# Kernel tuning notes

Measured on AMD Instinct MI355X. Metric: run time of the kernel, lower is better.

## Reference

```python
import jax, jax.numpy as jnp
import numpy as np

B = 16
Dv, Hv, Wv = 128, 128, 128   # patchsize voxel grid (C=1)
NPTS = 1920                  # 16*120 points
EPS_IN = 1e-5                # InstanceNorm eps


def _inorm(x):
    # InstanceNorm1d, affine=False: normalize over last (length) dim per (b, c)
    m = jnp.mean(x, axis=-1, keepdims=True)
    v = jnp.var(x, axis=-1, keepdims=True)
    return (x - m) * jax.lax.rsqrt(v + EPS_IN)


def _mlp(q, w1, b1, w2, b2, w3, b3, w4, b4, w5, b5):
    b = q.shape[0]
    x = q.reshape(b, 256, 8)                                    # (b, 2048//8, 8)
    x = jnp.einsum('bil,oi->bol', x, w1) + b1[None, :, None]    # Conv1d(256,240,1) -> (b,240,8)
    x = jax.nn.relu(_inorm(x.reshape(b, 64, 30)))               # view (b,64,30), IN(64)
    # Conv1d(64,128,1,groups=64): each in-ch -> 2 out-chs; then view (b,32,120)
    x = (x[:, :, None, :] * w2[None, :, :, None] + b2.reshape(1, 64, 2, 1)).reshape(b, 32, 120)
    x = jax.nn.relu(_inorm(x))
    # Conv1d(32,64,1,groups=32); view (b,16,480)
    x = (x[:, :, None, :] * w3[None, :, :, None] + b3.reshape(1, 32, 2, 1)).reshape(b, 16, 480)
    x = jax.nn.relu(_inorm(x))
    # Conv1d(16,64,1,groups=16); view (b,16,1920)
    x = (x[:, :, None, :] * w4[None, :, :, None] + b4.reshape(1, 16, 4, 1)).reshape(b, 16, 1920)
    x = jax.nn.relu(_inorm(x))
    return jnp.einsum('bil,oi->bol', x, w5) + b5[None, :, None]  # Conv1d(16,3,1) -> (b,3,1920)


def _splat(vals, grid):
    # True adjoint of 3D grid_sample (align_corners=False, zeros padding):
    # trilinear scatter-add of point values into the voxel grid.
    # vals: (b, N); grid: (b, N, 3) with (x, y, z) ~ (W, H, D) normalized coords.
    b, n = vals.shape
    px = ((grid[..., 0] + 1.0) * Wv - 1.0) * 0.5
    py = ((grid[..., 1] + 1.0) * Hv - 1.0) * 0.5
    pz = ((grid[..., 2] + 1.0) * Dv - 1.0) * 0.5
    x0f = jnp.floor(px); y0f = jnp.floor(py); z0f = jnp.floor(pz)
    fx = px - x0f; fy = py - y0f; fz = pz - z0f
    x0 = x0f.astype(jnp.int32); y0 = y0f.astype(jnp.int32); z0 = z0f.astype(jnp.int32)
    bidx = jnp.arange(b, dtype=jnp.int32)[:, None]
    out = jnp.zeros(b * Dv * Hv * Wv, dtype=vals.dtype)
    for dz in (0, 1):
        wz = fz if dz else (1.0 - fz)
        for dy in (0, 1):
            wy = fy if dy else (1.0 - fy)
            for dx in (0, 1):
                wx = fx if dx else (1.0 - fx)
                xi = x0 + dx; yi = y0 + dy; zi = z0 + dz
                w = wx * wy * wz * vals
                valid = (xi >= 0) & (xi < Wv) & (yi >= 0) & (yi < Hv) & (zi >= 0) & (zi < Dv)
                w = jnp.where(valid, w, 0.0)
                xi = jnp.clip(xi, 0, Wv - 1)
                yi = jnp.clip(yi, 0, Hv - 1)
                zi = jnp.clip(zi, 0, Dv - 1)
                flat = ((bidx * Dv + zi) * Hv + yi) * Wv + xi
                out = out.at[flat.ravel()].add(w.ravel())
    return out.reshape(b, 1, Dv, Hv, Wv)


def _avgpool3(x):
    # AvgPool3d(3, stride=1, padding=1, count_include_pad=True) as separable 1D averages
    for ax in (2, 3, 4):
        pad = [(1, 1) if i == ax else (0, 0) for i in range(5)]
        xp = jnp.pad(x, pad)
        n = x.shape[ax]
        x = (jax.lax.slice_in_dim(xp, 0, n, axis=ax)
             + jax.lax.slice_in_dim(xp, 1, n + 1, axis=ax)
             + jax.lax.slice_in_dim(xp, 2, n + 2, axis=ax)) / 3.0
    return x


def _smooth(x):
    return _avgpool3(_avgpool3(_avgpool3(x)))


def _forward(q, q_val, w1, b1, w2, b2, w3, b3, w4, b4, w5, b5):
    b = q.shape[0]
    q3 = _mlp(q, w1, b1, w2, b2, w3, b3, w4, b4, w5, b5)   # (b, 3, 1920)
    coords = jnp.tanh(q3)                                    # q0_coord
    grid = jnp.transpose(coords, (0, 2, 1))                  # (b, 1920, 3)
    vals = jnp.broadcast_to(jax.nn.sigmoid(q_val).reshape(1, NPTS), (b, NPTS))
    out = _splat(vals, grid)
    out0 = _splat(jnp.ones((b, NPTS), q.dtype), grid)
    return _smooth(out) / (_smooth(out0) + 0.001)


def setup_inputs() -> dict:
    key = jax.random.key(0)
    ks = jax.random.split(key, 12)
    sc = 0.1
    return {
        'q': jax.random.normal(ks[0], (B, 2048), jnp.float32),
        'q_val': jax.random.normal(ks[1], (1, 1, 16, 120), jnp.float32),
        'w1': jax.random.normal(ks[2], (240, 256), jnp.float32) * sc,
        'b1': jax.random.normal(ks[3], (240,), jnp.float32) * sc,
        'w2': jax.random.normal(ks[4], (64, 2), jnp.float32) * sc,
        'b2': jax.random.normal(ks[5], (128,), jnp.float32) * sc,
        'w3': jax.random.normal(ks[6], (32, 2), jnp.float32) * sc,
        'b3': jax.random.normal(ks[7], (64,), jnp.float32) * sc,
        'w4': jax.random.normal(ks[8], (16, 4), jnp.float32) * sc,
        'b4': jax.random.normal(ks[9], (64,), jnp.float32) * sc,
        'w5': jax.random.normal(ks[10], (3, 16), jnp.float32) * sc,
        'b5': jax.random.normal(ks[11], (3,), jnp.float32) * sc,
    }


def reference(q, q_val, w1, b1, w2, b2, w3, b3, w4, b4, w5, b5):
    return _forward(q, q_val, w1, b1, w2, b2, w3, b3, w4, b4, w5, b5)
```

## Files before the change

kernel.cpp:

```cpp
#include <hip/hip_runtime.h>
#include <cstddef>

#define NB 16
#define NVOX 128
#define NPT 1920
#define NPAIRS 32768

static __device__ __forceinline__ float2 f2(float a, float b) {
    float2 r; r.x = a; r.y = b; return r;
}

__global__ __launch_bounds__(256)
void zero_out(float4* __restrict__ out)
{
    int idx = blockIdx.x * 2048 + threadIdx.x;
    #pragma unroll
    for (int i = 0; i < 8; ++i)
        out[idx + i * 256] = make_float4(0.f, 0.f, 0.f, 0.f);
}

__global__ __launch_bounds__(256)
void mlp_stage1(const float* __restrict__ q, const float* __restrict__ w1,
                const float* __restrict__ b1, float* __restrict__ x1g)
{
    __shared__ float wrow[256];
    __shared__ float psum[256];
    const int o = blockIdx.x;
    const int t = threadIdx.x;

    wrow[t] = w1[o * 256 + t];
    __syncthreads();

    const int half = t >> 7;
    const int bl = t & 127;
    const int b = bl >> 3, l = bl & 7;
    const float* qb = q + b * 2048 + l + half * 1024;
    float s = 0.f;
    #pragma unroll 8
    for (int i = 0; i < 128; ++i)
        s = fmaf(wrow[half * 128 + i], qb[i * 8], s);
    psum[t] = s;
    __syncthreads();

    if (t < 128) {
        int bb = t >> 3, ll = t & 7;
        x1g[bb * 1920 + o * 8 + ll] = b1[o] + psum[t] + psum[t + 128];
    }
}

__global__ __launch_bounds__(256)
void mlp_tail(const float* __restrict__ x1g, const float* __restrict__ qval,
              const float* __restrict__ w2, const float* __restrict__ b2,
              const float* __restrict__ w3, const float* __restrict__ b3,
              const float* __restrict__ w4, const float* __restrict__ b4,
              const float* __restrict__ w5, const float* __restrict__ b5,
              float4* __restrict__ pts, unsigned char* __restrict__ flags)
{
    __shared__ float bufA[7680];
    __shared__ float bufC[3840];
    __shared__ float psum[256], psq[256];
    __shared__ float meanv[64], rstdv[64];
    __shared__ float m4[16], r4[16];

    const int b = blockIdx.x;
    const int t = threadIdx.x;

    for (int u = t; u < 1920; u += 256) bufA[u] = x1g[b * 1920 + u];
    __syncthreads();

    {
        int c = t >> 2, g = t & 3;
        float s = 0.f, s2 = 0.f;
        for (int p = g; p < 30; p += 4) { float v = bufA[c * 30 + p]; s += v; s2 += v * v; }
        psum[t] = s; psq[t] = s2;
    }
    __syncthreads();
    if (t < 64) {
        float s = 0.f, s2 = 0.f;
        for (int g = 0; g < 4; ++g) { s += psum[t * 4 + g]; s2 += psq[t * 4 + g]; }
        float m = s * (1.f / 30.f);
        float var = s2 * (1.f / 30.f) - m * m;
        meanv[t] = m; rstdv[t] = rsqrtf(var + 1e-5f);
    }
    __syncthreads();
    for (int k = t; k < 1920; k += 256) {
        int c = k / 30;
        bufA[k] = fmaxf((bufA[k] - meanv[c]) * rstdv[c], 0.f);
    }
    __syncthreads();

    for (int m = t; m < 3840; m += 256) {
        int c = m / 60;
        int r = m - c * 60;
        int j = r / 30;
        int p = r - j * 30;
        bufC[m] = fmaf(bufA[c * 30 + p], w2[c * 2 + j], b2[c * 2 + j]);
    }
    __syncthreads();
    {
        int c = t >> 3, g = t & 7;
        float s = 0.f, s2 = 0.f;
        for (int p = g; p < 120; p += 8) { float v = bufC[c * 120 + p]; s += v; s2 += v * v; }
        psum[t] = s; psq[t] = s2;
    }
    __syncthreads();
    if (t < 32) {
        float s = 0.f, s2 = 0.f;
        for (int g = 0; g < 8; ++g) { s += psum[t * 8 + g]; s2 += psq[t * 8 + g]; }
        float m = s * (1.f / 120.f);
        float var = s2 * (1.f / 120.f) - m * m;
        meanv[t] = m; rstdv[t] = rsqrtf(var + 1e-5f);
    }
    __syncthreads();
    for (int m = t; m < 3840; m += 256) {
        int c = m / 120;
        bufC[m] = fmaxf((bufC[m] - meanv[c]) * rstdv[c], 0.f);
    }
    __syncthreads();

    for (int m = t; m < 7680; m += 256) {
        int c = m / 240;
        int r = m - c * 240;
        int j = r / 120;
        int p = r - j * 120;
        bufA[m] = fmaf(bufC[c * 120 + p], w3[c * 2 + j], b3[c * 2 + j]);
    }
    __syncthreads();

    const int c3 = t >> 4, g3 = t & 15;
    {
        float s = 0.f, s2 = 0.f;
        for (int k = 0; k < 30; ++k) { float v = bufA[c3 * 480 + g3 + 16 * k]; s += v; s2 += v * v; }
        psum[t] = s; psq[t] = s2;
    }
    __syncthreads();
    if (t < 16) {
        float s = 0.f, s2 = 0.f;
        for (int g = 0; g < 16; ++g) { s += psum[t * 16 + g]; s2 += psq[t * 16 + g]; }
        float m = s * (1.f / 480.f);
        float var = s2 * (1.f / 480.f) - m * m;
        meanv[t] = m; rstdv[t] = rsqrtf(var + 1e-5f);
    }
    __syncthreads();
    {
        float m = meanv[c3], r = rstdv[c3];
        float s = 0.f, s2 = 0.f;
        for (int k = 0; k < 30; ++k) {
            int idx = c3 * 480 + g3 + 16 * k;
            float v = fmaxf((bufA[idx] - m) * r, 0.f);
            bufA[idx] = v; s += v; s2 += v * v;
        }
        psum[t] = s; psq[t] = s2;
    }
    __syncthreads();
    if (t < 16) {
        float s = 0.f, s2 = 0.f;
        for (int g = 0; g < 16; ++g) { s += psum[t * 16 + g]; s2 += psq[t * 16 + g]; }
        float sum4 = 0.f, sq4 = 0.f;
        for (int j = 0; j < 4; ++j) {
            float w = w4[t * 4 + j], bb = b4[t * 4 + j];
            sum4 += w * s + 480.f * bb;
            sq4  += w * w * s2 + 2.f * w * bb * s + 480.f * bb * bb;
        }
        float m = sum4 * (1.f / 1920.f);
        float var = sq4 * (1.f / 1920.f) - m * m;
        m4[t] = m; r4[t] = rsqrtf(var + 1e-5f);
    }
    __syncthreads();

    for (int l = t; l < NPT; l += 256) {
        int j = l / 480;
        int p = l - j * 480;
        float a0 = b5[0], a1 = b5[1], a2 = b5[2];
        #pragma unroll
        for (int c = 0; c < 16; ++c) {
            float xv = bufA[c * 480 + p];
            float x4 = fmaf(xv, w4[c * 4 + j], b4[c * 4 + j]);
            float h  = fmaxf((x4 - m4[c]) * r4[c], 0.f);
            a0 = fmaf(w5[c],      h, a0);
            a1 = fmaf(w5[16 + c], h, a1);
            a2 = fmaf(w5[32 + c], h, a2);
        }
        float px = tanhf(a0) * 64.f + 63.5f;
        float py = tanhf(a1) * 64.f + 63.5f;
        float pz = tanhf(a2) * 64.f + 63.5f;
        float val = 1.f / (1.f + expf(-qval[l]));

        float4 pv; pv.x = px; pv.y = py; pv.z = pz; pv.w = val;
        pts[b * NPT + l] = pv;

        int x0 = (int)floorf(px), y0 = (int)floorf(py), z0 = (int)floorf(pz);
        int xlo = max(0, x0 - 3), xhi = min(127, x0 + 4);
        int ylo = max(0, y0 - 3), yhi = min(127, y0 + 4);
        int zlo = max(0, z0 - 3), zhi = min(127, z0 + 4);
        if (xlo > xhi || ylo > yhi || zlo > zhi) continue;
        int txl = xlo >> 3, txh = xhi >> 3;
        int tyl = ylo >> 3, tyh = yhi >> 3;
        int tzl = zlo >> 3, tzh = zhi >> 3;
        for (int tz = tzl; tz <= tzh; ++tz)
            for (int ty = tyl; ty <= tyh; ++ty)
                for (int tx = txl; tx <= txh; ++tx)
                    flags[((b * 16 + tz) * 16 + ty) * 16 + tx] = 1;
    }
}

__global__ __launch_bounds__(256)
void compact_tiles(const unsigned char* __restrict__ flags,
                   int* __restrict__ count, int* __restrict__ list)
{
    int i = blockIdx.x * 256 + threadIdx.x;
    const unsigned short* fp = (const unsigned short*)flags;
    if (fp[i] != 0) {
        int pos = atomicAdd(count, 1);
        list[pos] = i;
    }
}

__device__ __forceinline__ void coef(int g, float& cm1, float& c0, float& cp1)
{
    cm1 = (g == 1 || g == 127) ? 5.f : 6.f;
    c0  = (g == 0 || g == 127) ? 4.f : 7.f;
    cp1 = (g == 0 || g == 126) ? 5.f : 6.f;
}

__global__ __launch_bounds__(512)
void tile_active(const float4* __restrict__ pts, const int* __restrict__ count,
                 const int* __restrict__ list, float* __restrict__ out)
{
    __shared__ float2 raw[14 * 14 * 22];
    __shared__ float2 zs[8 * 14 * 22];

    if ((int)blockIdx.x >= *count) return;
    const int code = list[blockIdx.x];
    const int pair = code & 7;
    const int ty   = (code >> 3) & 15;
    const int tz   = (code >> 7) & 15;
    const int b    = code >> 11;
    const int Tx = pair * 16, Ty = ty * 8, Tz = tz * 8;
    const int t = threadIdx.x;

    float* ob = out + (((size_t)(b * NVOX + Tz) * NVOX + Ty) * NVOX + Tx);

    for (int u = t; u < 14 * 14 * 22; u += 512) raw[u] = f2(0.f, 0.f);
    __syncthreads();

    const float4* pb = pts + b * NPT;
    for (int p = t; p < NPT; p += 512) {
        float4 pt = pb[p];
        float x0f = floorf(pt.x), y0f = floorf(pt.y), z0f = floorf(pt.z);
        int x0 = (int)x0f, y0 = (int)y0f, z0 = (int)z0f;
        int lx0 = x0 - Tx + 3, ly0 = y0 - Ty + 3, lz0 = z0 - Tz + 3;
        if (lx0 + 1 < 0 || lx0 > 21 || ly0 + 1 < 0 || ly0 > 13 ||
            lz0 + 1 < 0 || lz0 > 13) continue;
        float fx = pt.x - x0f, fy = pt.y - y0f, fz = pt.z - z0f;
        float val = pt.w;
        #pragma unroll
        for (int dz = 0; dz < 2; ++dz) {
            int zi = z0 + dz, lz = lz0 + dz;
            if ((unsigned)zi >= 128u || (unsigned)lz >= 14u) continue;
            float wz = dz ? fz : 1.f - fz;
            #pragma unroll
            for (int dy = 0; dy < 2; ++dy) {
                int yi = y0 + dy, ly = ly0 + dy;
                if ((unsigned)yi >= 128u || (unsigned)ly >= 14u) continue;
                float wy = dy ? fy : 1.f - fy;
                #pragma unroll
                for (int dx = 0; dx < 2; ++dx) {
                    int xi = x0 + dx, lx = lx0 + dx;
                    if ((unsigned)xi >= 128u || (unsigned)lx >= 22u) continue;
                    float w = (dx ? fx : 1.f - fx) * wy * wz;
                    float2* cell = &raw[(lz * 14 + ly) * 22 + lx];
                    atomicAdd(&cell->x, w * val);
                    atomicAdd(&cell->y, w);
                }
            }
        }
    }
    __syncthreads();

    for (int u = t; u < 8 * 14 * 22; u += 512) {
        int lx = u % 22;
        int tmp = u / 22;
        int ly = tmp % 14;
        int lz = tmp / 14;
        float cm1, c0, cp1; coef(Tz + lz, cm1, c0, cp1);
        const float2* a = &raw[(lz * 14 + ly) * 22 + lx];
        const int S = 14 * 22;
        float sx = (a[0].x + a[6 * S].x) + 3.f * (a[S].x + a[5 * S].x)
                 + cm1 * a[2 * S].x + c0 * a[3 * S].x + cp1 * a[4 * S].x;
        float sy = (a[0].y + a[6 * S].y) + 3.f * (a[S].y + a[5 * S].y)
                 + cm1 * a[2 * S].y + c0 * a[3 * S].y + cp1 * a[4 * S].y;
        zs[u] = f2(sx * (1.f / 27.f), sy * (1.f / 27.f));
    }
    __syncthreads();

    float2* ys = raw;
    for (int u = t; u < 8 * 8 * 22; u += 512) {
        int lx = u % 22;
        int tmp = u / 22;
        int ly = tmp % 8;
        int lz = tmp / 8;
        float cm1, c0, cp1; coef(Ty + ly, cm1, c0, cp1);
        const float2* a = &zs[(lz * 14 + ly) * 22 + lx];
        const int S = 22;
        float sx = (a[0].x + a[6 * S].x) + 3.f * (a[S].x + a[5 * S].x)
                 + cm1 * a[2 * S].x + c0 * a[3 * S].x + cp1 * a[4 * S].x;
        float sy = (a[0].y + a[6 * S].y) + 3.f * (a[S].y + a[5 * S].y)
                 + cm1 * a[2 * S].y + c0 * a[3 * S].y + cp1 * a[4 * S].y;
        ys[(lz * 8 + ly) * 22 + lx] = f2(sx * (1.f / 27.f), sy * (1.f / 27.f));
    }
    __syncthreads();

    for (int u = t; u < 16 * 8 * 8; u += 512) {
        int x = u & 15, y = (u >> 4) & 7, z = u >> 7;
        float cm1, c0, cp1; coef(Tx + x, cm1, c0, cp1);
        const float2* a = &ys[(z * 8 + y) * 22 + x];
        float sx = (a[0].x + a[6].x) + 3.f * (a[1].x + a[5].x)
                 + cm1 * a[2].x + c0 * a[3].x + cp1 * a[4].x;
        float sy = (a[0].y + a[6].y) + 3.f * (a[1].y + a[5].y)
                 + cm1 * a[2].y + c0 * a[3].y + cp1 * a[4].y;
        ob[((size_t)z * NVOX + y) * NVOX + x] =
            (sx * (1.f / 27.f)) / (sy * (1.f / 27.f) + 0.001f);
    }
}

extern "C" void kernel_launch(void* const* d_in, const int* in_sizes, int n_in,
                              void* d_out, int out_size, void* d_ws, size_t ws_size,
                              hipStream_t stream)
{
    const float* q    = (const float*)d_in[0];
    const float* qval = (const float*)d_in[1];
    const float* w1   = (const float*)d_in[2];
    const float* b1   = (const float*)d_in[3];
    const float* w2   = (const float*)d_in[4];
    const float* b2   = (const float*)d_in[5];
    const float* w3   = (const float*)d_in[6];
    const float* b3   = (const float*)d_in[7];
    const float* w4   = (const float*)d_in[8];
    const float* b4   = (const float*)d_in[9];
    const float* w5   = (const float*)d_in[10];
    const float* b5   = (const float*)d_in[11];
    float* out = (float*)d_out;

    unsigned char* flags = (unsigned char*)d_ws;
    int*    count = (int*)((char*)d_ws + 65536);
    int*    list  = (int*)((char*)d_ws + 65552);
    float4* pts   = (float4*)((char*)d_ws + 196624);
    float*  x1g   = (float*)((char*)d_ws + 688144);

    hipMemsetAsync(d_ws, 0, 65540, stream);

    zero_out<<<4096, 256, 0, stream>>>((float4*)out);

    mlp_stage1<<<240, 256, 0, stream>>>(q, w1, b1, x1g);

    mlp_tail<<<NB, 256, 0, stream>>>(x1g, qval, w2, b2, w3, b3,
                                     w4, b4, w5, b5, pts, flags);

    compact_tiles<<<NPAIRS / 256, 256, 0, stream>>>(flags, count, list);

    tile_active<<<NPAIRS, 512, 0, stream>>>(pts, count, list, out);
}
```

Before: 252.1 us.

## Bin points per tile via count/scan/fill and fuse zeroing into tile kernel

Replaces the active-tile flag list with a per-tile point binning scheme. Counts are accumulated atomically, a single-block prefix scan produces offsets, and a fill kernel scatters points into per-tile bins, so each tile block reads only its own points instead of scanning all 1920 points of its batch. The separate output zeroing kernel is removed: empty tiles write zeros directly. The separable smoothing is restructured into register-blocked in-place passes with float4 stores, which drops the second shared buffer. The cost is extra kernels (a serial one-block scan and the fill) plus global atomics on cursors.

```diff
diff --git a/kernel.cpp b/kernel.cpp
--- a/kernel.cpp
+++ b/kernel.cpp
@@ -8,15 +8,6 @@
 
 static __device__ __forceinline__ float2 f2(float a, float b) {
     float2 r; r.x = a; r.y = b; return r;
-}
-
-__global__ __launch_bounds__(256)
-void zero_out(float4* __restrict__ out)
-{
-    int idx = blockIdx.x * 2048 + threadIdx.x;
-    #pragma unroll
-    for (int i = 0; i < 8; ++i)
-        out[idx + i * 256] = make_float4(0.f, 0.f, 0.f, 0.f);
 }
 
 __global__ __launch_bounds__(256)
@@ -48,13 +39,22 @@
     }
 }
 
+__device__ __forceinline__ void bin_range(int x0, int y0, int z0,
+                                          int& pxl, int& pxh, int& tyl, int& tyh,
+                                          int& tzl, int& tzh)
+{
+    pxl = max(0, x0 - 3) >> 4; pxh = min(127, x0 + 4) >> 4;
+    tyl = max(0, y0 - 3) >> 3; tyh = min(127, y0 + 4) >> 3;
+    tzl = max(0, z0 - 3) >> 3; tzh = min(127, z0 + 4) >> 3;
+}
+
 __global__ __launch_bounds__(256)
 void mlp_tail(const float* __restrict__ x1g, const float* __restrict__ qval,
               const float* __restrict__ w2, const float* __restrict__ b2,
               const float* __restrict__ w3, const float* __restrict__ b3,
               const float* __restrict__ w4, const float* __restrict__ b4,
               const float* __restrict__ w5, const float* __restrict__ b5,
-              float4* __restrict__ pts, unsigned char* __restrict__ flags)
+              float4* __restrict__ pts, int* __restrict__ counts)
 {
     __shared__ float bufA[7680];
     __shared__ float bufC[3840];
@@ -190,30 +190,60 @@
         pts[b * NPT + l] = pv;
 
         int x0 = (int)floorf(px), y0 = (int)floorf(py), z0 = (int)floorf(pz);
-        int xlo = max(0, x0 - 3), xhi = min(127, x0 + 4);
-        int ylo = max(0, y0 - 3), yhi = min(127, y0 + 4);
-        int zlo = max(0, z0 - 3), zhi = min(127, z0 + 4);
-        if (xlo > xhi || ylo > yhi || zlo > zhi) continue;
-        int txl = xlo >> 3, txh = xhi >> 3;
-        int tyl = ylo >> 3, tyh = yhi >> 3;
-        int tzl = zlo >> 3, tzh = zhi >> 3;
+        int pxl, pxh, tyl, tyh, tzl, tzh;
+        bin_range(x0, y0, z0, pxl, pxh, tyl, tyh, tzl, tzh);
         for (int tz = tzl; tz <= tzh; ++tz)
             for (int ty = tyl; ty <= tyh; ++ty)
-                for (int tx = txl; tx <= txh; ++tx)
-                    flags[((b * 16 + tz) * 16 + ty) * 16 + tx] = 1;
-    }
+                for (int px_ = pxl; px_ <= pxh; ++px_)
+                    atomicAdd(&counts[((b * 16 + tz) * 16 + ty) * 8 + px_], 1);
+    }
+}
+
+__global__ __launch_bounds__(1024)
+void scan32k(const int* __restrict__ counts, int* __restrict__ offsets,
+             int* __restrict__ cursors)
+{
+    __shared__ int part[1024];
+    const int t = threadIdx.x;
+    int s = 0;
+    int local[32];
+    #pragma unroll
+    for (int i = 0; i < 32; ++i) { local[i] = counts[t * 32 + i]; s += local[i]; }
+    part[t] = s;
+    __syncthreads();
+    for (int off = 1; off < 1024; off <<= 1) {
+        int v = (t >= off) ? part[t - off] : 0;
+        __syncthreads();
+        part[t] += v;
+        __syncthreads();
+    }
+    int running = part[t] - s;
+    #pragma unroll
+    for (int i = 0; i < 32; ++i) {
+        offsets[t * 32 + i] = running;
+        cursors[t * 32 + i] = running;
+        running += local[i];
+    }
+    if (t == 1023) offsets[32768] = running;
 }
 
 __global__ __launch_bounds__(256)
-void compact_tiles(const unsigned char* __restrict__ flags,
-                   int* __restrict__ count, int* __restrict__ list)
+void bin_fill(const float4* __restrict__ pts, int* __restrict__ cursors,
+              float4* __restrict__ binned)
 {
     int i = blockIdx.x * 256 + threadIdx.x;
-    const unsigned short* fp = (const unsigned short*)flags;
-    if (fp[i] != 0) {
-        int pos = atomicAdd(count, 1);
-        list[pos] = i;
-    }
+    int b = i / NPT;
+    float4 pt = pts[i];
+    int x0 = (int)floorf(pt.x), y0 = (int)floorf(pt.y), z0 = (int)floorf(pt.z);
+    int pxl, pxh, tyl, tyh, tzl, tzh;
+    bin_range(x0, y0, z0, pxl, pxh, tyl, tyh, tzl, tzh);
+    for (int tz = tzl; tz <= tzh; ++tz)
+        for (int ty = tyl; ty <= tyh; ++ty)
+            for (int px_ = pxl; px_ <= pxh; ++px_) {
+                int bin = ((b * 16 + tz) * 16 + ty) * 8 + px_;
+                int pos = atomicAdd(&cursors[bin], 1);
+                binned[pos] = pt;
+            }
 }
 
 __device__ __forceinline__ void coef(int g, float& cm1, float& c0, float& cp1)
@@ -223,15 +253,13 @@
     cp1 = (g == 0 || g == 126) ? 5.f : 6.f;
 }
 
-__global__ __launch_bounds__(512)
-void tile_active(const float4* __restrict__ pts, const int* __restrict__ count,
-                 const int* __restrict__ list, float* __restrict__ out)
-{
-    __shared__ float2 raw[14 * 14 * 22];
-    __shared__ float2 zs[8 * 14 * 22];
-
-    if ((int)blockIdx.x >= *count) return;
-    const int code = list[blockIdx.x];
+__global__ __launch_bounds__(256)
+void tile_smooth(const float4* __restrict__ binned,
+                 const int* __restrict__ offsets, float* __restrict__ out)
+{
+    __shared__ __align__(16) float2 raw[14 * 14 * 22];
+
+    const int code = blockIdx.x;
     const int pair = code & 7;
     const int ty   = (code >> 3) & 15;
     const int tz   = (code >> 7) & 15;
@@ -239,19 +267,30 @@
     const int Tx = pair * 16, Ty = ty * 8, Tz = tz * 8;
     const int t = threadIdx.x;
 
+    const int off = offsets[code];
+    const int n   = offsets[code + 1] - off;
+
     float* ob = out + (((size_t)(b * NVOX + Tz) * NVOX + Ty) * NVOX + Tx);
 
-    for (int u = t; u < 14 * 14 * 22; u += 512) raw[u] = f2(0.f, 0.f);
-    __syncthreads();
-
-    const float4* pb = pts + b * NPT;
-    for (int p = t; p < NPT; p += 512) {
-        float4 pt = pb[p];
+    if (n == 0) {
+        int z = t >> 5, y = (t >> 2) & 7, qx = t & 3;
+        *(float4*)(ob + ((size_t)z * NVOX + y) * NVOX + qx * 4) =
+            make_float4(0.f, 0.f, 0.f, 0.f);
+        return;
+    }
+
+    {
+        float4* r4p = (float4*)raw;
+        for (int u = t; u < 14 * 14 * 11; u += 256)
+            r4p[u] = make_float4(0.f, 0.f, 0.f, 0.f);
+    }
+    __syncthreads();
+
+    for (int p = t; p < n; p += 256) {
+        float4 pt = binned[off + p];
         float x0f = floorf(pt.x), y0f = floorf(pt.y), z0f = floorf(pt.z);
         int x0 = (int)x0f, y0 = (int)y0f, z0 = (int)z0f;
         int lx0 = x0 - Tx + 3, ly0 = y0 - Ty + 3, lz0 = z0 - Tz + 3;
-        if (lx0 + 1 < 0 || lx0 > 21 || ly0 + 1 < 0 || ly0 > 13 ||
-            lz0 + 1 < 0 || lz0 > 13) continue;
         float fx = pt.x - x0f, fy = pt.y - y0f, fz = pt.z - z0f;
         float val = pt.w;
         #pragma unroll
@@ -278,49 +317,60 @@
     }
     __syncthreads();
 
-    for (int u = t; u < 8 * 14 * 22; u += 512) {
-        int lx = u % 22;
-        int tmp = u / 22;
-        int ly = tmp % 14;
-        int lz = tmp / 14;
-        float cm1, c0, cp1; coef(Tz + lz, cm1, c0, cp1);
-        const float2* a = &raw[(lz * 14 + ly) * 22 + lx];
-        const int S = 14 * 22;
-        float sx = (a[0].x + a[6 * S].x) + 3.f * (a[S].x + a[5 * S].x)
-                 + cm1 * a[2 * S].x + c0 * a[3 * S].x + cp1 * a[4 * S].x;
-        float sy = (a[0].y + a[6 * S].y) + 3.f * (a[S].y + a[5 * S].y)
-                 + cm1 * a[2 * S].y + c0 * a[3 * S].y + cp1 * a[4 * S].y;
-        zs[u] = f2(sx * (1.f / 27.f), sy * (1.f / 27.f));
-    }
-    __syncthreads();
-
-    float2* ys = raw;
-    for (int u = t; u < 8 * 8 * 22; u += 512) {
-        int lx = u % 22;
-        int tmp = u / 22;
-        int ly = tmp % 8;
-        int lz = tmp / 8;
-        float cm1, c0, cp1; coef(Ty + ly, cm1, c0, cp1);
-        const float2* a = &zs[(lz * 14 + ly) * 22 + lx];
-        const int S = 22;
-        float sx = (a[0].x + a[6 * S].x) + 3.f * (a[S].x + a[5 * S].x)
-                 + cm1 * a[2 * S].x + c0 * a[3 * S].x + cp1 * a[4 * S].x;
-        float sy = (a[0].y + a[6 * S].y) + 3.f * (a[S].y + a[5 * S].y)
-                 + cm1 * a[2 * S].y + c0 * a[3 * S].y + cp1 * a[4 * S].y;
-        ys[(lz * 8 + ly) * 22 + lx] = f2(sx * (1.f / 27.f), sy * (1.f / 27.f));
-    }
-    __syncthreads();
-
-    for (int u = t; u < 16 * 8 * 8; u += 512) {
-        int x = u & 15, y = (u >> 4) & 7, z = u >> 7;
-        float cm1, c0, cp1; coef(Tx + x, cm1, c0, cp1);
-        const float2* a = &ys[(z * 8 + y) * 22 + x];
-        float sx = (a[0].x + a[6].x) + 3.f * (a[1].x + a[5].x)
-                 + cm1 * a[2].x + c0 * a[3].x + cp1 * a[4].x;
-        float sy = (a[0].y + a[6].y) + 3.f * (a[1].y + a[5].y)
-                 + cm1 * a[2].y + c0 * a[3].y + cp1 * a[4].y;
-        ob[((size_t)z * NVOX + y) * NVOX + x] =
-            (sx * (1.f / 27.f)) / (sy * (1.f / 27.f) + 0.001f);
+    for (int cc = t; cc < 14 * 22; cc += 256) {
+        int ly = cc / 22, lx = cc - ly * 22;
+        float2 v[14];
+        #pragma unroll
+        for (int j = 0; j < 14; ++j) v[j] = raw[(j * 14 + ly) * 22 + lx];
+        #pragma unroll
+        for (int k = 0; k < 8; ++k) {
+            float cm1, c0, cp1; coef(Tz + k, cm1, c0, cp1);
+            float sx = (v[k].x + v[k + 6].x) + 3.f * (v[k + 1].x + v[k + 5].x)
+                     + cm1 * v[k + 2].x + c0 * v[k + 3].x + cp1 * v[k + 4].x;
+            float sy = (v[k].y + v[k + 6].y) + 3.f * (v[k + 1].y + v[k + 5].y)
+                     + cm1 * v[k + 2].y + c0 * v[k + 3].y + cp1 * v[k + 4].y;
+            raw[((k + 3) * 14 + ly) * 22 + lx] = f2(sx * (1.f / 27.f), sy * (1.f / 27.f));
+        }
+    }
+    __syncthreads();
+
+    if (t < 8 * 22) {
+        int lz = t / 22, lx = t - lz * 22;
+        float2 v[14];
+        #pragma unroll
+        for (int j = 0; j < 14; ++j) v[j] = raw[((lz + 3) * 14 + j) * 22 + lx];
+        #pragma unroll
+        for (int k = 0; k < 8; ++k) {
+            float cm1, c0, cp1; coef(Ty + k, cm1, c0, cp1);
+            float sx = (v[k].x + v[k + 6].x) + 3.f * (v[k + 1].x + v[k + 5].x)
+                     + cm1 * v[k + 2].x + c0 * v[k + 3].x + cp1 * v[k + 4].x;
+            float sy = (v[k].y + v[k + 6].y) + 3.f * (v[k + 1].y + v[k + 5].y)
+                     + cm1 * v[k + 2].y + c0 * v[k + 3].y + cp1 * v[k + 4].y;
+            raw[((lz + 3) * 14 + (k + 3)) * 22 + lx] = f2(sx * (1.f / 27.f), sy * (1.f / 27.f));
+        }
+    }
+    __syncthreads();
+
+    {
+        int row = t >> 2, qx = t & 3;
+        int z = row >> 3, y = row & 7;
+        const float2* base = &raw[((z + 3) * 14 + (y + 3)) * 22];
+        float2 m[10];
+        #pragma unroll
+        for (int j = 0; j < 10; ++j) m[j] = base[4 * qx + j];
+        float4 res;
+        float* rp = (float*)&res;
+        #pragma unroll
+        for (int xi = 0; xi < 4; ++xi) {
+            int gx = Tx + 4 * qx + xi;
+            float cm1, c0, cp1; coef(gx, cm1, c0, cp1);
+            float sx = (m[xi].x + m[xi + 6].x) + 3.f * (m[xi + 1].x + m[xi + 5].x)
+                     + cm1 * m[xi + 2].x + c0 * m[xi + 3].x + cp1 * m[xi + 4].x;
+            float sy = (m[xi].y + m[xi + 6].y) + 3.f * (m[xi + 1].y + m[xi + 5].y)
+                     + cm1 * m[xi + 2].y + c0 * m[xi + 3].y + cp1 * m[xi + 4].y;
+            rp[xi] = (sx * (1.f / 27.f)) / (sy * (1.f / 27.f) + 0.001f);
+        }
+        *(float4*)(ob + ((size_t)z * NVOX + y) * NVOX + qx * 4) = res;
     }
 }
 
@@ -342,22 +392,23 @@
     const float* b5   = (const float*)d_in[11];
     float* out = (float*)d_out;
 
-    unsigned char* flags = (unsigned char*)d_ws;
-    int*    count = (int*)((char*)d_ws + 65536);
-    int*    list  = (int*)((char*)d_ws + 65552);
-    float4* pts   = (float4*)((char*)d_ws + 196624);
-    float*  x1g   = (float*)((char*)d_ws + 688144);
-
-    hipMemsetAsync(d_ws, 0, 65540, stream);
-
-    zero_out<<<4096, 256, 0, stream>>>((float4*)out);
+    int*    counts  = (int*)d_ws;
+    int*    offsets = (int*)((char*)d_ws + 0x040000);
+    int*    cursors = (int*)((char*)d_ws + 0x080000);
+    float4* pts     = (float4*)((char*)d_ws + 0x0C0000);
+    float4* binned  = (float4*)((char*)d_ws + 0x140000);
+    float*  x1g     = (float*)((char*)d_ws + 0x600000);
+
+    hipMemsetAsync(counts, 0, 32768 * sizeof(int), stream);
 
     mlp_stage1<<<240, 256, 0, stream>>>(q, w1, b1, x1g);
 
     mlp_tail<<<NB, 256, 0, stream>>>(x1g, qval, w2, b2, w3, b3,
-                                     w4, b4, w5, b5, pts, flags);
-
-    compact_tiles<<<NPAIRS / 256, 256, 0, stream>>>(flags, count, list);
-
-    tile_active<<<NPAIRS, 512, 0, stream>>>(pts, count, list, out);
-}
+                                     w4, b4, w5, b5, pts, counts);
+
+    scan32k<<<1, 1024, 0, stream>>>(counts, offsets, cursors);
+
+    bin_fill<<<(NB * NPT) / 256, 256, 0, stream>>>(pts, cursors, binned);
+
+    tile_smooth<<<NPAIRS, 256, 0, stream>>>(binned, offsets, out);
+}
```

Measured after the change: 345.9 us. 37.2% more time.
